# Optimization experiments

Measured on AMD Instinct MI355X. Metric: run time of the kernel, lower is better.

The kernel has to match this reference:

```python
import jax, jax.numpy as jnp
import numpy as np

B, C, R = 100000, 64, 128

def setup_inputs() -> dict:
    key = jax.random.key(0)
    k1, k2, k3 = jax.random.split(key, 3)
    return {
        "compressed_vectors": jax.random.normal(k1, (B, C, 3), dtype=jnp.float32),
        "W1": jax.random.normal(k2, (C, 32), dtype=jnp.float32) * (1.0 / np.sqrt(C)),
        "b1": jnp.zeros((32,), dtype=jnp.float32),
        "W2": jax.random.normal(k3, (32, R * C), dtype=jnp.float32) * (1.0 / np.sqrt(32)),
        "b2": jnp.zeros((R * C,), dtype=jnp.float32),
    }

def reference(compressed_vectors, W1, b1, W2, b2):
    # scalar invariants: L2 norm over Cartesian axis -> [B, C]
    scalar_invariants = jnp.linalg.norm(compressed_vectors, axis=-1)
    # tiny MLP: C -> 32 -> R*C
    h = jax.nn.relu(scalar_invariants @ W1 + b1)
    scalar_weights = (h @ W2 + b2).reshape(-1, R, C)  # [B, R, C]
    # outer product of vectors: [B, C, 3, 3]
    rank2_tensors = jnp.einsum('bci,bcj->bcij', compressed_vectors, compressed_vectors)
    # weighted bilinear contraction over channels: [B, R, 3, 3]
    reconstructed_tensors = jnp.einsum('brc,bcij->brij', scalar_weights, rank2_tensors)
    return reconstructed_tensors
```

## Files before the change

### kernel.cpp

```cpp
#include <hip/hip_runtime.h>
#include <hip/hip_bf16.h>


#define NB 16
#define RT 8

typedef float f32x4 __attribute__((ext_vector_type(4)));
typedef __bf16 bf16x8 __attribute__((ext_vector_type(8)));

static __device__ __forceinline__ unsigned short bf_bits(float f) {
  __hip_bfloat16 h = __float2bfloat16(f);
  return *reinterpret_cast<const unsigned short*>(&h);
}
static __device__ __forceinline__ unsigned int pack_bf2(float a, float b) {
  return (unsigned int)bf_bits(a) | ((unsigned int)bf_bits(b) << 16);
}

__global__ void prep_w2t(const float* __restrict__ W2, unsigned short* __restrict__ w2t) {
  int rc = blockIdx.x * 256 + threadIdx.x;
  unsigned int u[16];
#pragma unroll
  for (int kp = 0; kp < 16; ++kp) {
    float a = W2[(size_t)(2 * kp) * 8192 + rc];
    float b = W2[(size_t)(2 * kp + 1) * 8192 + rc];
    u[kp] = pack_bf2(a, b);
  }
  unsigned int* dst = reinterpret_cast<unsigned int*>(w2t + (size_t)rc * 32);
#pragma unroll
  for (int j = 0; j < 16; ++j) dst[j] = u[j];
}

__global__ __launch_bounds__(256, 4)
void erl_main(const float* __restrict__ v, const float* __restrict__ W1,
              const float* __restrict__ b1, const float* __restrict__ b2,
              const unsigned short* __restrict__ w2t, float* __restrict__ out) {
  __shared__ __align__(16) char smem[24064];
  unsigned short* W_lds = reinterpret_cast<unsigned short*>(smem);
  float* W1_lds = reinterpret_cast<float*>(smem);
  float* s_lds = reinterpret_cast<float*>(smem + 18688);
  unsigned short* h_lds = reinterpret_cast<unsigned short*>(smem + 23040);

  const int t = threadIdx.x;
  const int b0 = blockIdx.x * NB;
  const int lane = t & 63;
  const int wid = t >> 6;
  const int x = lane >> 4;
  const int col = lane & 15;

  {
    const f32x4* w1v = reinterpret_cast<const f32x4*>(W1);
    f32x4* w1d = reinterpret_cast<f32x4*>(W1_lds);
    w1d[t] = w1v[t];
    w1d[t + 256] = w1v[t + 256];
  }
#pragma unroll
  for (int j = 0; j < 4; ++j) {
    int p = t + j * 256;
    int b = p >> 6, c = p & 63;
    const float* vp = v + ((size_t)(b0 + b) * 64 + c) * 3;
    float vx = vp[0], vy = vp[1], vz = vp[2];
    s_lds[b * 68 + c] = sqrtf(vx * vx + vy * vy + vz * vz);
  }

  const int seff = (col < 9) ? col : 8;
  const int ei = seff / 3;
  const int ej = seff - ei * 3;
  bf16x8 mfr[4][2];
#pragma unroll
  for (int i = 0; i < 4; ++i) {
    int b = wid * 4 + i;
#pragma unroll
    for (int ch = 0; ch < 2; ++ch) {
      const float* vb = v + ((size_t)(b0 + b) * 64 + ch * 32 + x * 8) * 3;
      union { f32x4 q[6]; float f[24]; } u;
#pragma unroll
      for (int l = 0; l < 6; ++l) u.q[l] = reinterpret_cast<const f32x4*>(vb)[l];
      bf16x8 fr;
#pragma unroll
      for (int e = 0; e < 8; ++e) {
        float vx = u.f[e * 3 + 0], vy = u.f[e * 3 + 1], vz = u.f[e * 3 + 2];
        float pa = (ei == 0) ? vx : ((ei == 1) ? vy : vz);
        float pb = (ej == 0) ? vx : ((ej == 1) ? vy : vz);
        fr[e] = (__bf16)(pa * pb);
      }
      mfr[i][ch] = fr;
    }
  }
  __syncthreads();

  {
    int b = t >> 4, kk = t & 15;
    float a0 = b1[kk], a1 = b1[kk + 16];
    const f32x4* srow = reinterpret_cast<const f32x4*>(s_lds + b * 68);
#pragma unroll
    for (int c4 = 0; c4 < 16; ++c4) {
      f32x4 sv = srow[c4];
#pragma unroll
      for (int uu = 0; uu < 4; ++uu) {
        int c = c4 * 4 + uu;
        a0 = fmaf(sv[uu], W1_lds[c * 32 + kk], a0);
        a1 = fmaf(sv[uu], W1_lds[c * 32 + kk + 16], a1);
      }
    }
    h_lds[b * 32 + kk] = bf_bits(fmaxf(a0, 0.f));
    h_lds[b * 32 + kk + 16] = bf_bits(fmaxf(a1, 0.f));
  }
  __syncthreads();

  bf16x8 hfrag = *reinterpret_cast<const bf16x8*>(&h_lds[col * 32 + x * 8]);

  const unsigned short* ap0 = w2t + (size_t)wid * 4096 + col * 32 + x * 8;
  const unsigned short* ap1 = ap0 + 2048;
  const float* b2p = b2 + wid * 128 + x * 4;
  const int w_widx = col * 584 + wid * 144 + x * 4;
  const int w_ridx = wid * 4 * 584 + (col & 7) * 72 + x * 8;
  float* op[4];
#pragma unroll
  for (int i = 0; i < 4; ++i)
    op[i] = out + (size_t)(b0 + wid * 4 + i) * 1152 + x * 36 + col;
  const bool do_store = (x < 2) && (col < 9);

  for (int rt = 0; rt < 128 / RT; ++rt) {
#pragma unroll
    for (int half = 0; half < 2; ++half) {
      const unsigned short* ap = half ? ap1 : ap0;
      bf16x8 af[4];
      f32x4 acc1[4];
#pragma unroll
      for (int i = 0; i < 4; ++i) {
        af[i] = *reinterpret_cast<const bf16x8*>(ap + i * 512);
        acc1[i] = *reinterpret_cast<const f32x4*>(b2p + half * 64 + i * 16);
      }
#pragma unroll
      for (int i = 0; i < 4; ++i) {
        acc1[i] = __builtin_amdgcn_mfma_f32_16x16x32_bf16(af[i], hfrag, acc1[i], 0, 0, 0);
        unsigned int* wp = reinterpret_cast<unsigned int*>(&W_lds[w_widx + half * 72 + i * 16]);
        wp[0] = pack_bf2(acc1[i][0], acc1[i][1]);
        wp[1] = pack_bf2(acc1[i][2], acc1[i][3]);
      }
    }
    ap0 += 16384; ap1 += 16384; b2p += 512;
    __syncthreads();

#pragma unroll
    for (int i = 0; i < 4; ++i) {
      f32x4 acc2 = {0.f, 0.f, 0.f, 0.f};
#pragma unroll
      for (int ch = 0; ch < 2; ++ch) {
        bf16x8 a2 = *reinterpret_cast<const bf16x8*>(&W_lds[w_ridx + i * 584 + ch * 32]);
        acc2 = __builtin_amdgcn_mfma_f32_16x16x32_bf16(a2, mfr[i][ch], acc2, 0, 0, 0);
      }
      if (do_store) {
        float* p = op[i];
#pragma unroll
        for (int q = 0; q < 4; ++q) p[q * 9] = acc2[q];
      }
      op[i] += 72;
    }
    __syncthreads();
  }
}

extern "C" void kernel_launch(void* const* d_in, const int* in_sizes, int n_in,
                              void* d_out, int out_size, void* d_ws, size_t ws_size,
                              hipStream_t stream) {
  const float* v  = (const float*)d_in[0];
  const float* W1 = (const float*)d_in[1];
  const float* b1 = (const float*)d_in[2];
  const float* W2 = (const float*)d_in[3];
  const float* b2 = (const float*)d_in[4];
  float* out = (float*)d_out;

  unsigned short* w2t = (unsigned short*)d_ws;

  prep_w2t<<<32, 256, 0, stream>>>(W2, w2t);
  erl_main<<<100000 / NB, 256, 0, stream>>>(v, W1, b1, b2, w2t, out);
}
```

Baseline: 403.8 us.

## Double r-tile width and software-pipeline W2 fragment loads across chunks

Processes 16 output ranks per outer iteration instead of 8, which halves the number of barrier pairs and lets the second MFMA stage use all 16 output rows of each tile, so every x lane now stores. W2 fragments and bias for the next chunk are prefetched into registers before the current chunk's MFMAs, including across the barrier into the next r-tile. LDS grows to about 37 KB and register pressure rises, which may cut occupancy below the 4-block launch bound. An extra barrier is added before the W tile area is overwritten, since the LDS layout now overlaps h_lds and s_lds with W_lds.

```diff
diff --git a/kernel.cpp b/kernel.cpp
--- a/kernel.cpp
+++ b/kernel.cpp
@@ -3,7 +3,7 @@
 
 
 #define NB 16
-#define RT 8
+#define RT 16
 
 typedef float f32x4 __attribute__((ext_vector_type(4)));
 typedef __bf16 bf16x8 __attribute__((ext_vector_type(8)));
@@ -34,11 +34,11 @@
 void erl_main(const float* __restrict__ v, const float* __restrict__ W1,
               const float* __restrict__ b1, const float* __restrict__ b2,
               const unsigned short* __restrict__ w2t, float* __restrict__ out) {
-  __shared__ __align__(16) char smem[24064];
+  __shared__ __align__(16) char smem[37376];
   unsigned short* W_lds = reinterpret_cast<unsigned short*>(smem);
   float* W1_lds = reinterpret_cast<float*>(smem);
-  float* s_lds = reinterpret_cast<float*>(smem + 18688);
-  unsigned short* h_lds = reinterpret_cast<unsigned short*>(smem + 23040);
+  float* s_lds = reinterpret_cast<float*>(smem + 8192);
+  unsigned short* h_lds = reinterpret_cast<unsigned short*>(smem + 12544);
 
   const int t = threadIdx.x;
   const int b0 = blockIdx.x * NB;
@@ -108,54 +108,73 @@
   __syncthreads();
 
   bf16x8 hfrag = *reinterpret_cast<const bf16x8*>(&h_lds[col * 32 + x * 8]);
+  __syncthreads();
 
-  const unsigned short* ap0 = w2t + (size_t)wid * 4096 + col * 32 + x * 8;
-  const unsigned short* ap1 = ap0 + 2048;
-  const float* b2p = b2 + wid * 128 + x * 4;
-  const int w_widx = col * 584 + wid * 144 + x * 4;
-  const int w_ridx = wid * 4 * 584 + (col & 7) * 72 + x * 8;
+  const unsigned short* ap = w2t + (size_t)wid * 8192 + col * 32 + x * 8;
+  const float* b2p = b2 + wid * 256 + x * 4;
+  const int w_widx = col * 1168 + wid * 288 + x * 4;
+  const int w_ridx = wid * 4672 + col * 72 + x * 8;
   float* op[4];
 #pragma unroll
   for (int i = 0; i < 4; ++i)
     op[i] = out + (size_t)(b0 + wid * 4 + i) * 1152 + x * 36 + col;
-  const bool do_store = (x < 2) && (col < 9);
+  const bool do_store = (col < 9);
 
-  for (int rt = 0; rt < 128 / RT; ++rt) {
+  bf16x8 afA[4], afB[4];
+  f32x4 bsA[4];
 #pragma unroll
-    for (int half = 0; half < 2; ++half) {
-      const unsigned short* ap = half ? ap1 : ap0;
-      bf16x8 af[4];
-      f32x4 acc1[4];
+  for (int jj = 0; jj < 4; ++jj) {
+    afA[jj] = *reinterpret_cast<const bf16x8*>(ap + jj * 512);
+    bsA[jj] = *reinterpret_cast<const f32x4*>(b2p + jj * 16);
+  }
+
+  for (int rt = 0; rt < 8; ++rt) {
 #pragma unroll
-      for (int i = 0; i < 4; ++i) {
-        af[i] = *reinterpret_cast<const bf16x8*>(ap + i * 512);
-        acc1[i] = *reinterpret_cast<const f32x4*>(b2p + half * 64 + i * 16);
+    for (int ck = 0; ck < 4; ++ck) {
+      if (ck < 3) {
+#pragma unroll
+        for (int jj = 0; jj < 4; ++jj) {
+          int tt = (ck + 1) * 4 + jj;
+          afB[jj] = *reinterpret_cast<const bf16x8*>(ap + tt * 512);
+        }
       }
 #pragma unroll
-      for (int i = 0; i < 4; ++i) {
-        acc1[i] = __builtin_amdgcn_mfma_f32_16x16x32_bf16(af[i], hfrag, acc1[i], 0, 0, 0);
-        unsigned int* wp = reinterpret_cast<unsigned int*>(&W_lds[w_widx + half * 72 + i * 16]);
-        wp[0] = pack_bf2(acc1[i][0], acc1[i][1]);
-        wp[1] = pack_bf2(acc1[i][2], acc1[i][3]);
+      for (int jj = 0; jj < 4; ++jj) {
+        f32x4 acc = (ck == 0) ? bsA[jj]
+                  : *reinterpret_cast<const f32x4*>(b2p + (ck * 4 + jj) * 16);
+        acc = __builtin_amdgcn_mfma_f32_16x16x32_bf16(afA[jj], hfrag, acc, 0, 0, 0);
+        unsigned int* wp = reinterpret_cast<unsigned int*>(&W_lds[w_widx + ck * 72 + jj * 16]);
+        wp[0] = pack_bf2(acc[0], acc[1]);
+        wp[1] = pack_bf2(acc[2], acc[3]);
+      }
+      if (ck < 3) {
+#pragma unroll
+        for (int jj = 0; jj < 4; ++jj) afA[jj] = afB[jj];
       }
     }
-    ap0 += 16384; ap1 += 16384; b2p += 512;
+    ap += 32768; b2p += 1024;
     __syncthreads();
+
+    if (rt < 7) {
+#pragma unroll
+      for (int jj = 0; jj < 4; ++jj) {
+        afA[jj] = *reinterpret_cast<const bf16x8*>(ap + jj * 512);
+        bsA[jj] = *reinterpret_cast<const f32x4*>(b2p + jj * 16);
+      }
+    }
 
 #pragma unroll
     for (int i = 0; i < 4; ++i) {
+      bf16x8 a20 = *reinterpret_cast<const bf16x8*>(&W_lds[w_ridx + i * 1168]);
+      bf16x8 a21 = *reinterpret_cast<const bf16x8*>(&W_lds[w_ridx + i * 1168 + 32]);
       f32x4 acc2 = {0.f, 0.f, 0.f, 0.f};
-#pragma unroll
-      for (int ch = 0; ch < 2; ++ch) {
-        bf16x8 a2 = *reinterpret_cast<const bf16x8*>(&W_lds[w_ridx + i * 584 + ch * 32]);
-        acc2 = __builtin_amdgcn_mfma_f32_16x16x32_bf16(a2, mfr[i][ch], acc2, 0, 0, 0);
-      }
+      acc2 = __builtin_amdgcn_mfma_f32_16x16x32_bf16(a20, mfr[i][0], acc2, 0, 0, 0);
+      acc2 = __builtin_amdgcn_mfma_f32_16x16x32_bf16(a21, mfr[i][1], acc2, 0, 0, 0);
       if (do_store) {
         float* p = op[i];
-#pragma unroll
-        for (int q = 0; q < 4; ++q) p[q * 9] = acc2[q];
+        p[0] = acc2[0]; p[9] = acc2[1]; p[18] = acc2[2]; p[27] = acc2[3];
       }
-      op[i] += 72;
+      op[i] += 144;
     }
     __syncthreads();
   }
```

Measured after the change: 401.5 us. No clear change (-0.6%).

## Give each wave a private r-slice, drop block barriers, stage outputs for coalesced stores

Applied to the files above, without the earlier changes.

Restructures the main loop so each wave owns a 32-row slice of R for all 16 batch elements, using a private LDS scratch region. This replaces the per-tile __syncthreads with wave-local lgkmcnt waits. W2 fragments are double-buffered in registers to prefetch the next group. The input vectors and W1 (transposed) are staged through LDS, and the rank-2 products are built once in LDS and loaded into 32 fragments per lane. Outputs are staged in LDS and written as contiguous 36-word rows. Larger LDS use and register pressure cut occupancy (launch bounds drop from 4 to 2 blocks per CU), and reusing the scratch region for outputs within a wave relies on the waits being sufficient.

```diff
diff --git a/kernel.cpp b/kernel.cpp
--- a/kernel.cpp
+++ b/kernel.cpp
@@ -3,10 +3,10 @@
 
 
 #define NB 16
-#define RT 8
 
 typedef float f32x4 __attribute__((ext_vector_type(4)));
 typedef __bf16 bf16x8 __attribute__((ext_vector_type(8)));
+typedef unsigned int u32x4 __attribute__((ext_vector_type(4)));
 
 static __device__ __forceinline__ unsigned short bf_bits(float f) {
   __hip_bfloat16 h = __float2bfloat16(f);
@@ -14,6 +14,9 @@
 }
 static __device__ __forceinline__ unsigned int pack_bf2(float a, float b) {
   return (unsigned int)bf_bits(a) | ((unsigned int)bf_bits(b) << 16);
+}
+static __device__ __forceinline__ bf16x8 as_bf16x8(u32x4 u) {
+  union { u32x4 u; bf16x8 b; } c; c.u = u; return c.b;
 }
 
 __global__ void prep_w2t(const float* __restrict__ W2, unsigned short* __restrict__ w2t) {
@@ -30,76 +33,61 @@
   for (int j = 0; j < 16; ++j) dst[j] = u[j];
 }
 
-__global__ __launch_bounds__(256, 4)
+__global__ __launch_bounds__(256, 2)
 void erl_main(const float* __restrict__ v, const float* __restrict__ W1,
               const float* __restrict__ b1, const float* __restrict__ b2,
               const unsigned short* __restrict__ w2t, float* __restrict__ out) {
-  __shared__ __align__(16) char smem[24064];
-  unsigned short* W_lds = reinterpret_cast<unsigned short*>(smem);
-  float* W1_lds = reinterpret_cast<float*>(smem);
-  float* s_lds = reinterpret_cast<float*>(smem + 18688);
-  unsigned short* h_lds = reinterpret_cast<unsigned short*>(smem + 23040);
+  __shared__ __align__(16) char smem[47104];
+  float* v_lds = reinterpret_cast<float*>(smem);
+  unsigned short* M_lds = reinterpret_cast<unsigned short*>(smem + 12288);
+  float* W1T = reinterpret_cast<float*>(smem + 33024);
+  float* s_lds = reinterpret_cast<float*>(smem + 41728);
+  unsigned short* h_lds = reinterpret_cast<unsigned short*>(smem + 46080);
 
   const int t = threadIdx.x;
+  const int wid = t >> 6, lane = t & 63;
+  const int x = lane >> 4, col = lane & 15;
   const int b0 = blockIdx.x * NB;
-  const int lane = t & 63;
-  const int wid = t >> 6;
-  const int x = lane >> 4;
-  const int col = lane & 15;
 
   {
-    const f32x4* w1v = reinterpret_cast<const f32x4*>(W1);
-    f32x4* w1d = reinterpret_cast<f32x4*>(W1_lds);
-    w1d[t] = w1v[t];
-    w1d[t + 256] = w1v[t + 256];
+    const f32x4* src = reinterpret_cast<const f32x4*>(v + (size_t)b0 * 192);
+    f32x4* dst = reinterpret_cast<f32x4*>(v_lds);
+    dst[t] = src[t]; dst[t + 256] = src[t + 256]; dst[t + 512] = src[t + 512];
+#pragma unroll
+    for (int j = 0; j < 8; ++j) {
+      int p = t + j * 256;
+      W1T[(p & 31) * 68 + (p >> 5)] = W1[p];
+    }
   }
+  __syncthreads();
+
 #pragma unroll
   for (int j = 0; j < 4; ++j) {
     int p = t + j * 256;
     int b = p >> 6, c = p & 63;
-    const float* vp = v + ((size_t)(b0 + b) * 64 + c) * 3;
-    float vx = vp[0], vy = vp[1], vz = vp[2];
+    float vx = v_lds[p * 3], vy = v_lds[p * 3 + 1], vz = v_lds[p * 3 + 2];
     s_lds[b * 68 + c] = sqrtf(vx * vx + vy * vy + vz * vz);
-  }
-
-  const int seff = (col < 9) ? col : 8;
-  const int ei = seff / 3;
-  const int ej = seff - ei * 3;
-  bf16x8 mfr[4][2];
-#pragma unroll
-  for (int i = 0; i < 4; ++i) {
-    int b = wid * 4 + i;
-#pragma unroll
-    for (int ch = 0; ch < 2; ++ch) {
-      const float* vb = v + ((size_t)(b0 + b) * 64 + ch * 32 + x * 8) * 3;
-      union { f32x4 q[6]; float f[24]; } u;
-#pragma unroll
-      for (int l = 0; l < 6; ++l) u.q[l] = reinterpret_cast<const f32x4*>(vb)[l];
-      bf16x8 fr;
-#pragma unroll
-      for (int e = 0; e < 8; ++e) {
-        float vx = u.f[e * 3 + 0], vy = u.f[e * 3 + 1], vz = u.f[e * 3 + 2];
-        float pa = (ei == 0) ? vx : ((ei == 1) ? vy : vz);
-        float pb = (ej == 0) ? vx : ((ej == 1) ? vy : vz);
-        fr[e] = (__bf16)(pa * pb);
-      }
-      mfr[i][ch] = fr;
-    }
+    unsigned short* mp = M_lds + b * 648 + c;
+    unsigned short pxx = bf_bits(vx * vx), pxy = bf_bits(vx * vy), pxz = bf_bits(vx * vz);
+    unsigned short pyy = bf_bits(vy * vy), pyz = bf_bits(vy * vz), pzz = bf_bits(vz * vz);
+    mp[0] = pxx; mp[72] = pxy; mp[144] = pxz;
+    mp[216] = pxy; mp[288] = pyy; mp[360] = pyz;
+    mp[432] = pxz; mp[504] = pyz; mp[576] = pzz;
   }
   __syncthreads();
 
   {
     int b = t >> 4, kk = t & 15;
     float a0 = b1[kk], a1 = b1[kk + 16];
-    const f32x4* srow = reinterpret_cast<const f32x4*>(s_lds + b * 68);
 #pragma unroll
     for (int c4 = 0; c4 < 16; ++c4) {
-      f32x4 sv = srow[c4];
+      f32x4 sv = *reinterpret_cast<const f32x4*>(s_lds + b * 68 + c4 * 4);
+      f32x4 w0 = *reinterpret_cast<const f32x4*>(W1T + kk * 68 + c4 * 4);
+      f32x4 w1 = *reinterpret_cast<const f32x4*>(W1T + (kk + 16) * 68 + c4 * 4);
 #pragma unroll
-      for (int uu = 0; uu < 4; ++uu) {
-        int c = c4 * 4 + uu;
-        a0 = fmaf(sv[uu], W1_lds[c * 32 + kk], a0);
-        a1 = fmaf(sv[uu], W1_lds[c * 32 + kk + 16], a1);
+      for (int u = 0; u < 4; ++u) {
+        a0 = fmaf(sv[u], w0[u], a0);
+        a1 = fmaf(sv[u], w1[u], a1);
       }
     }
     h_lds[b * 32 + kk] = bf_bits(fmaxf(a0, 0.f));
@@ -108,56 +96,80 @@
   __syncthreads();
 
   bf16x8 hfrag = *reinterpret_cast<const bf16x8*>(&h_lds[col * 32 + x * 8]);
+  const int seff = (col < 9) ? col : 8;
+  bf16x8 mfr[16][2];
+#pragma unroll
+  for (int b = 0; b < 16; ++b) {
+#pragma unroll
+    for (int ch = 0; ch < 2; ++ch)
+      mfr[b][ch] = *reinterpret_cast<const bf16x8*>(&M_lds[b * 648 + seff * 72 + ch * 32 + x * 8]);
+  }
+  __syncthreads();
 
-  const unsigned short* ap0 = w2t + (size_t)wid * 4096 + col * 32 + x * 8;
-  const unsigned short* ap1 = ap0 + 2048;
-  const float* b2p = b2 + wid * 128 + x * 4;
-  const int w_widx = col * 584 + wid * 144 + x * 4;
-  const int w_ridx = wid * 4 * 584 + (col & 7) * 72 + x * 8;
-  float* op[4];
+  unsigned int* Wu = reinterpret_cast<unsigned int*>(smem + wid * 9472);
+
+  const int rbase0 = wid * 32;
+  const unsigned short* ap = w2t + ((size_t)rbase0 * 64 + col) * 32 + x * 8;
+  const float* b2p = b2 + rbase0 * 64 + x * 4;
+  const int wwr_u = col * 148 + x * 2;
+  const int wrd_u = (col & 3) * 36 + x * 4;
+  unsigned int* outu = reinterpret_cast<unsigned int*>(out) + (size_t)b0 * 1152 + wid * 288 + lane;
+  const bool ostore = (x == 0) && (col < 9);
+
+  bf16x8 afA[4], afB[4];
 #pragma unroll
-  for (int i = 0; i < 4; ++i)
-    op[i] = out + (size_t)(b0 + wid * 4 + i) * 1152 + x * 36 + col;
-  const bool do_store = (x < 2) && (col < 9);
+  for (int j = 0; j < 4; ++j) afA[j] = *reinterpret_cast<const bf16x8*>(ap + j * 512);
 
-  for (int rt = 0; rt < 128 / RT; ++rt) {
+  for (int it = 0; it < 8; ++it) {
 #pragma unroll
-    for (int half = 0; half < 2; ++half) {
-      const unsigned short* ap = half ? ap1 : ap0;
-      bf16x8 af[4];
-      f32x4 acc1[4];
+    for (int g = 0; g < 4; ++g) {
+      if (g < 3) {
 #pragma unroll
-      for (int i = 0; i < 4; ++i) {
-        af[i] = *reinterpret_cast<const bf16x8*>(ap + i * 512);
-        acc1[i] = *reinterpret_cast<const f32x4*>(b2p + half * 64 + i * 16);
+        for (int j = 0; j < 4; ++j)
+          afB[j] = *reinterpret_cast<const bf16x8*>(ap + ((g + 1) * 4 + j) * 512);
+      } else if (it < 7) {
+#pragma unroll
+        for (int j = 0; j < 4; ++j)
+          afB[j] = *reinterpret_cast<const bf16x8*>(ap + 8192 + j * 512);
       }
 #pragma unroll
-      for (int i = 0; i < 4; ++i) {
-        acc1[i] = __builtin_amdgcn_mfma_f32_16x16x32_bf16(af[i], hfrag, acc1[i], 0, 0, 0);
-        unsigned int* wp = reinterpret_cast<unsigned int*>(&W_lds[w_widx + half * 72 + i * 16]);
-        wp[0] = pack_bf2(acc1[i][0], acc1[i][1]);
-        wp[1] = pack_bf2(acc1[i][2], acc1[i][3]);
+      for (int j = 0; j < 4; ++j) {
+        int tt = g * 4 + j;
+        f32x4 acc = *reinterpret_cast<const f32x4*>(b2p + tt * 16);
+        acc = __builtin_amdgcn_mfma_f32_16x16x32_bf16(afA[j], hfrag, acc, 0, 0, 0);
+        unsigned int* wp = &Wu[wwr_u + (tt >> 2) * 36 + (tt & 3) * 8];
+        wp[0] = pack_bf2(acc[0], acc[1]);
+        wp[1] = pack_bf2(acc[2], acc[3]);
+      }
+      afA[0] = afB[0]; afA[1] = afB[1]; afA[2] = afB[2]; afA[3] = afB[3];
+    }
+    ap += 8192; b2p += 256;
+
+    asm volatile("s_waitcnt lgkmcnt(0)" ::: "memory");
+
+#pragma unroll
+    for (int b = 0; b < 16; ++b) {
+      bf16x8 a0 = as_bf16x8(*reinterpret_cast<const u32x4*>(&Wu[b * 148 + wrd_u]));
+      bf16x8 a1 = as_bf16x8(*reinterpret_cast<const u32x4*>(&Wu[b * 148 + wrd_u + 16]));
+      f32x4 o = {0.f, 0.f, 0.f, 0.f};
+      o = __builtin_amdgcn_mfma_f32_16x16x32_bf16(a0, mfr[b][0], o, 0, 0, 0);
+      o = __builtin_amdgcn_mfma_f32_16x16x32_bf16(a1, mfr[b][1], o, 0, 0, 0);
+      if (ostore) {
+        unsigned int* od = &Wu[b * 36 + col];
+        od[0]  = __float_as_uint(o[0]);
+        od[9]  = __float_as_uint(o[1]);
+        od[18] = __float_as_uint(o[2]);
+        od[27] = __float_as_uint(o[3]);
       }
     }
-    ap0 += 16384; ap1 += 16384; b2p += 512;
-    __syncthreads();
 
+    asm volatile("s_waitcnt lgkmcnt(0)" ::: "memory");
+
+    if (lane < 36) {
 #pragma unroll
-    for (int i = 0; i < 4; ++i) {
-      f32x4 acc2 = {0.f, 0.f, 0.f, 0.f};
-#pragma unroll
-      for (int ch = 0; ch < 2; ++ch) {
-        bf16x8 a2 = *reinterpret_cast<const bf16x8*>(&W_lds[w_ridx + i * 584 + ch * 32]);
-        acc2 = __builtin_amdgcn_mfma_f32_16x16x32_bf16(a2, mfr[i][ch], acc2, 0, 0, 0);
-      }
-      if (do_store) {
-        float* p = op[i];
-#pragma unroll
-        for (int q = 0; q < 4; ++q) p[q * 9] = acc2[q];
-      }
-      op[i] += 72;
+      for (int b = 0; b < 16; ++b)
+        outu[(size_t)b * 1152 + it * 36] = Wu[b * 36 + lane];
     }
-    __syncthreads();
   }
 }
 
```

Measured after the change: 461.6 us. +14.3%, slower.
